# Optimization experiments

Measured on AMD Instinct MI355X. Metric: run time of the kernel, lower is better.

Reference implementation:

```python
import jax, jax.numpy as jnp
import numpy as np

N = 1024
EMB = 128
FC = 512


def setup_inputs() -> dict:
    key = jax.random.key(0)
    ks = jax.random.split(key, 13)
    s = 0.05
    return {
        "x": jax.random.normal(ks[0], (N, 2), jnp.float32),
        "w_rel0": jax.random.normal(ks[1], (EMB, 2), jnp.float32) * s,
        "b_rel0": jax.random.normal(ks[2], (EMB,), jnp.float32) * s,
        "w_root0": jax.random.normal(ks[3], (EMB, 2), jnp.float32) * s,
        "w_rel1": jax.random.normal(ks[4], (EMB, EMB), jnp.float32) * s,
        "b_rel1": jax.random.normal(ks[5], (EMB,), jnp.float32) * s,
        "w_root1": jax.random.normal(ks[6], (EMB, EMB), jnp.float32) * s,
        "lw0": jax.random.normal(ks[7], (FC, EMB), jnp.float32) * s,
        "lb0": jax.random.normal(ks[8], (FC,), jnp.float32) * s,
        "lw1": jax.random.normal(ks[9], (FC, FC), jnp.float32) * s,
        "lb1": jax.random.normal(ks[10], (FC,), jnp.float32) * s,
        "lw2": jax.random.normal(ks[11], (1, FC), jnp.float32) * s,
        "lb2": jax.random.normal(ks[12], (1,), jnp.float32) * s,
    }


def _sage(x, w_rel, b_rel, w_root):
    # DenseSAGEConv with adj = all-ones NxN: neighbor mean == global mean.
    # out = lin_rel(adj@x / deg) + lin_root(x); lin_root has no bias.
    agg = jnp.mean(x, axis=0, keepdims=True)            # (1, d_in)
    return agg @ w_rel.T + b_rel + x @ w_root.T          # (N, d_out)


def reference(x, w_rel0, b_rel0, w_root0, w_rel1, b_rel1, w_root1,
              lw0, lb0, lw1, lb1, lw2, lb2):
    h = jax.nn.relu(_sage(x, w_rel0, b_rel0, w_root0))    # (N, EMB)
    h = jax.nn.relu(_sage(h, w_rel1, b_rel1, w_root1))    # (N, EMB)
    # triu(ones, 1).nonzero() -> all pairs i < j (static, N known at trace time)
    ei, ej = np.triu_indices(h.shape[0], 1)
    e = h[ei] * h[ej]                                     # (E, EMB)
    o = jax.nn.relu(e @ lw0.T + lb0)                      # (E, FC)
    o = jax.nn.relu(o @ lw1.T + lb1)                      # (E, FC)
    o = o @ lw2.T + lb2                                   # (E, 1)
    return jax.nn.sigmoid(o)[:, 0]                        # (E,)
```

## Files before the change

### kernel.cpp

```cpp
#include <hip/hip_runtime.h>
#include <hip/hip_bf16.h>
#include <math.h>

#define NN 1024
#define EMB 128
#define FC 512
#define NEDGE 523776
#define BM 64

typedef __attribute__((ext_vector_type(16))) float f32x16;
typedef __attribute__((ext_vector_type(8))) short bf16x8;
typedef __attribute__((ext_vector_type(4))) unsigned int u32x4;
typedef __attribute__((ext_vector_type(8))) int i32x8;

__device__ __forceinline__ float bf2f(unsigned short u) {
  union { unsigned int i; float f; } v; v.i = ((unsigned int)u) << 16; return v.f;
}
__device__ __forceinline__ unsigned short f2bf(float f) {
  return __builtin_bit_cast(unsigned short, __float2bfloat16(f));
}
__device__ __forceinline__ int cum_edges(int i) { return i * NN - ((i * (i + 1)) >> 1); }

__device__ __forceinline__ unsigned int pk4_fp8(float a, float b, float c, float d) {
  int v = __builtin_amdgcn_cvt_pk_fp8_f32(a, b, 0, false);
  v = __builtin_amdgcn_cvt_pk_fp8_f32(c, d, v, true);
  return (unsigned int)v;
}
#define MFMA32_L0(A,B,C) __builtin_amdgcn_mfma_scale_f32_32x32x64_f8f6f4((A),(B),(C),0,0,0,0x76767676,0,0x7f7f7f7f)
#define MFMA32_L1(A,B,C) __builtin_amdgcn_mfma_scale_f32_32x32x64_f8f6f4((A),(B),(C),0,0,0,0x72727272,0,0x7f7f7f7f)

__global__ void k_cvt_weights(const float* __restrict__ lw0, const float* __restrict__ lw1,
                              unsigned int* __restrict__ w0q, unsigned int* __restrict__ w1q) {
  int d = blockIdx.x * 256 + threadIdx.x;
  if (d < 16384) {
    int dw = d & 7, lane = (d >> 3) & 63, f = (d >> 9) & 1, kb = (d >> 10) & 1, wv = (d >> 11) & 7;
    int fc = wv*64 + f*32 + (lane & 31);
    int k  = kb*64 + (lane >> 5)*32 + dw*4;
    float4 s = *(const float4*)(lw0 + fc*EMB + k);
    w0q[d] = pk4_fp8(s.x*64.f, s.y*64.f, s.z*64.f, s.w*64.f);
  } else {
    int u = d - 16384;
    int dw = u & 7, lane = (u >> 3) & 63, f = (u >> 9) & 1, kb = (u >> 10) & 7, wv = (u >> 13) & 7;
    int fc = wv*64 + f*32 + (lane & 31);
    int k  = kb*64 + (lane >> 5)*32 + dw*4;
    float4 s = *(const float4*)(lw1 + fc*FC + k);
    w1q[u] = pk4_fp8(s.x*64.f, s.y*64.f, s.z*64.f, s.w*64.f);
  }
}

__global__ void k_mean_x(const float* __restrict__ x, float* __restrict__ mean0) {
  __shared__ float sx[256], sy[256];
  float ax = 0.f, ay = 0.f;
  for (int i = threadIdx.x; i < NN; i += 256) { ax += x[2*i]; ay += x[2*i+1]; }
  sx[threadIdx.x] = ax; sy[threadIdx.x] = ay;
  __syncthreads();
  for (int st = 128; st > 0; st >>= 1) {
    if (threadIdx.x < st) { sx[threadIdx.x] += sx[threadIdx.x+st]; sy[threadIdx.x] += sy[threadIdx.x+st]; }
    __syncthreads();
  }
  if (threadIdx.x == 0) { mean0[0] = sx[0] * (1.f/NN); mean0[1] = sy[0] * (1.f/NN); }
}

__global__ void k_sage0(const float* __restrict__ x, const float* __restrict__ wrel,
                        const float* __restrict__ brel, const float* __restrict__ wroot,
                        const float* __restrict__ mean0, float* __restrict__ h0) {
  int idx = blockIdx.x * 256 + threadIdx.x;
  int i = idx >> 7, c = idx & 127;
  float v = mean0[0]*wrel[2*c] + mean0[1]*wrel[2*c+1] + brel[c]
          + x[2*i]*wroot[2*c] + x[2*i+1]*wroot[2*c+1];
  h0[idx] = fmaxf(v, 0.f);
}

__global__ void k_mean_h0(const float* __restrict__ h0, float* __restrict__ mean1) {
  __shared__ float s[256];
  int c = blockIdx.x;
  float a = 0.f;
  for (int i = threadIdx.x; i < NN; i += 256) a += h0[i*EMB + c];
  s[threadIdx.x] = a;
  __syncthreads();
  for (int st = 128; st > 0; st >>= 1) {
    if (threadIdx.x < st) s[threadIdx.x] += s[threadIdx.x+st];
    __syncthreads();
  }
  if (threadIdx.x == 0) mean1[c] = s[0] * (1.f/NN);
}

__global__ void k_relc(const float* __restrict__ mean1, const float* __restrict__ wrel1,
                       const float* __restrict__ brel1, float* __restrict__ relc) {
  int c = threadIdx.x;
  float a = brel1[c];
  #pragma unroll 8
  for (int k = 0; k < EMB; ++k) a += mean1[k] * wrel1[c*EMB + k];
  relc[c] = a;
}

__global__ void k_sage1(const float* __restrict__ h0, const float* __restrict__ wroot1,
                        const float* __restrict__ relc, unsigned short* __restrict__ hb) {
  int idx = blockIdx.x * 256 + threadIdx.x;
  int i = idx >> 7, c = idx & 127;
  const float4* hr = (const float4*)(h0 + i*EMB);
  const float4* wr = (const float4*)(wroot1 + c*EMB);
  float a = relc[c];
  #pragma unroll 8
  for (int k = 0; k < EMB/4; ++k) {
    float4 h = hr[k], w = wr[k];
    a += h.x*w.x + h.y*w.y + h.z*w.z + h.w*w.w;
  }
  hb[idx] = f2bf(fmaxf(a, 0.f) * 32.0f);
}

__global__ __launch_bounds__(512, 4)
void k_edge_mlp(const unsigned short* __restrict__ hb,
                const unsigned int* __restrict__ w0q,
                const float* __restrict__ lb0,
                const unsigned int* __restrict__ w1q,
                const float* __restrict__ lb1,
                const float* __restrict__ lw2,
                const float* __restrict__ lb2,
                float* __restrict__ out) {
  __shared__ __align__(16) unsigned int e_lds[2048];
  __shared__ __align__(16) unsigned int o0_lds[8192];

  const int tid  = threadIdx.x;
  const int lane = tid & 63;
  const int wv   = tid >> 6;
  const int l31  = lane & 31;
  const int hi   = lane >> 5;
  const int blk  = blockIdx.x;
  const int fcb  = wv * 64;

  const char* w0w = (const char*)w0q + wv * 8192;
  const char* w1w = (const char*)w1q + wv * 32768;

  {
    int r = tid >> 3, q = tid & 7;
    int k = blk * BM + r;
    float s = sqrtf((float)(4190209 - 8*k));
    int i = (int)((2047.0f - s) * 0.5f);
    if (i < 0) i = 0;
    if (i > NN-2) i = NN-2;
    if (cum_edges(i+1) <= k) ++i;
    if (cum_edges(i+1) <= k) ++i;
    if (cum_edges(i) > k) --i;
    if (cum_edges(i) > k) --i;
    int j = k - cum_edges(i) + i + 1;
    const bf16x8* hi8 = (const bf16x8*)(hb + i*EMB + q*16);
    const bf16x8* hj8 = (const bf16x8*)(hb + j*EMB + q*16);
    float p[16];
    #pragma unroll
    for (int g = 0; g < 2; ++g) {
      bf16x8 a = hi8[g], b = hj8[g];
      #pragma unroll
      for (int u = 0; u < 8; ++u)
        p[g*8+u] = bf2f((unsigned short)a[u]) * bf2f((unsigned short)b[u]);
    }
    u32x4 d;
    #pragma unroll
    for (int u = 0; u < 4; ++u)
      d[u] = pk4_fp8(p[4*u], p[4*u+1], p[4*u+2], p[4*u+3]);
    int byt = (r>>5)*4096 + (q>>2)*2048 + (q&1)*1024 + (((q>>1)&1)*32 + (r&31))*16;
    *(u32x4*)((char*)e_lds + byt) = d;
  }
  __syncthreads();

  f32x16 acc[2][2];

  #pragma unroll
  for (int f = 0; f < 2; ++f)
    #pragma unroll
    for (int t = 0; t < 4; ++t) {
      float4 bv = *(const float4*)(lb0 + fcb + f*32 + t*8 + hi*4);
      #pragma unroll
      for (int e = 0; e < 2; ++e) {
        acc[e][f][4*t+0] = bv.x*128.f; acc[e][f][4*t+1] = bv.y*128.f;
        acc[e][f][4*t+2] = bv.z*128.f; acc[e][f][4*t+3] = bv.w*128.f;
      }
    }
  {
    const char* rbe = (const char*)e_lds + lane*16;
    #pragma unroll
    for (int kb = 0; kb < 2; ++kb) {
      i32x8 a0 = *(const i32x8*)(w0w + (kb*2+0)*2048 + lane*32);
      i32x8 a1 = *(const i32x8*)(w0w + (kb*2+1)*2048 + lane*32);
      i32x8 b0, b1;
      *(u32x4*)&b0       = *(const u32x4*)(rbe + kb*2048);
      *((u32x4*)&b0 + 1) = *(const u32x4*)(rbe + kb*2048 + 1024);
      *(u32x4*)&b1       = *(const u32x4*)(rbe + 4096 + kb*2048);
      *((u32x4*)&b1 + 1) = *(const u32x4*)(rbe + 4096 + kb*2048 + 1024);
      __builtin_amdgcn_s_setprio(1);
      acc[0][0] = MFMA32_L0(a0, b0, acc[0][0]);
      acc[0][1] = MFMA32_L0(a1, b0, acc[0][1]);
      acc[1][0] = MFMA32_L0(a0, b1, acc[1][0]);
      acc[1][1] = MFMA32_L0(a1, b1, acc[1][1]);
      __builtin_amdgcn_s_setprio(0);
    }
  }

  {
    char* ob = (char*)o0_lds + wv*2048 + l31*16 + hi*4;
    #pragma unroll
    for (int f = 0; f < 2; ++f)
      #pragma unroll
      for (int e = 0; e < 2; ++e)
        #pragma unroll
        for (int t = 0; t < 4; ++t) {
          unsigned int d = pk4_fp8(fmaxf(acc[e][f][4*t+0], 0.f),
                                   fmaxf(acc[e][f][4*t+1], 0.f),
                                   fmaxf(acc[e][f][4*t+2], 0.f),
                                   fmaxf(acc[e][f][4*t+3], 0.f));
          *(unsigned int*)(ob + e*16384 + (t>>1)*1024 + f*512 + (t&1)*8) = d;
        }
  }
  __syncthreads();

  #pragma unroll
  for (int f = 0; f < 2; ++f)
    #pragma unroll
    for (int t = 0; t < 4; ++t) {
      float4 bv = *(const float4*)(lb1 + fcb + f*32 + t*8 + hi*4);
      #pragma unroll
      for (int e = 0; e < 2; ++e) {
        acc[e][f][4*t+0] = bv.x; acc[e][f][4*t+1] = bv.y;
        acc[e][f][4*t+2] = bv.z; acc[e][f][4*t+3] = bv.w;
      }
    }
  {
    const char* rbo = (const char*)o0_lds + lane*16;
    #pragma unroll
    for (int kb = 0; kb < 8; ++kb) {
      i32x8 a0 = *(const i32x8*)(w1w + (kb*2+0)*2048 + lane*32);
      i32x8 a1 = *(const i32x8*)(w1w + (kb*2+1)*2048 + lane*32);
      i32x8 b0, b1;
      *(u32x4*)&b0       = *(const u32x4*)(rbo + kb*2048);
      *((u32x4*)&b0 + 1) = *(const u32x4*)(rbo + kb*2048 + 1024);
      *(u32x4*)&b1       = *(const u32x4*)(rbo + 16384 + kb*2048);
      *((u32x4*)&b1 + 1) = *(const u32x4*)(rbo + 16384 + kb*2048 + 1024);
      __builtin_amdgcn_s_setprio(1);
      acc[0][0] = MFMA32_L1(a0, b0, acc[0][0]);
      acc[0][1] = MFMA32_L1(a1, b0, acc[0][1]);
      acc[1][0] = MFMA32_L1(a0, b1, acc[1][0]);
      acc[1][1] = MFMA32_L1(a1, b1, acc[1][1]);
      __builtin_amdgcn_s_setprio(0);
    }
  }

  {
    float rs0 = 0.f, rs1 = 0.f;
    #pragma unroll
    for (int f = 0; f < 2; ++f)
      #pragma unroll
      for (int t = 0; t < 4; ++t) {
        float4 l2v = *(const float4*)(lw2 + fcb + f*32 + t*8 + hi*4);
        rs0 += fmaxf(acc[0][f][4*t+0], 0.f) * l2v.x;
        rs0 += fmaxf(acc[0][f][4*t+1], 0.f) * l2v.y;
        rs0 += fmaxf(acc[0][f][4*t+2], 0.f) * l2v.z;
        rs0 += fmaxf(acc[0][f][4*t+3], 0.f) * l2v.w;
        rs1 += fmaxf(acc[1][f][4*t+0], 0.f) * l2v.x;
        rs1 += fmaxf(acc[1][f][4*t+1], 0.f) * l2v.y;
        rs1 += fmaxf(acc[1][f][4*t+2], 0.f) * l2v.z;
        rs1 += fmaxf(acc[1][f][4*t+3], 0.f) * l2v.w;
      }
    rs0 += __shfl_xor(rs0, 32, 64);
    rs1 += __shfl_xor(rs1, 32, 64);
    float* red = (float*)e_lds;
    if (hi == 0) {
      red[wv*64 + l31]      = rs0;
      red[wv*64 + 32 + l31] = rs1;
    }
  }
  __syncthreads();

  if (tid < BM) {
    const float* red = (const float*)e_lds;
    float v = lb2[0];
    #pragma unroll
    for (int w = 0; w < 8; ++w) v += red[w*BM + tid];
    out[blk*BM + tid] = 1.0f / (1.0f + __expf(-v));
  }
}

extern "C" void kernel_launch(void* const* d_in, const int* in_sizes, int n_in,
                              void* d_out, int out_size, void* d_ws, size_t ws_size,
                              hipStream_t stream) {
  const float* x      = (const float*)d_in[0];
  const float* wrel0  = (const float*)d_in[1];
  const float* brel0  = (const float*)d_in[2];
  const float* wroot0 = (const float*)d_in[3];
  const float* wrel1  = (const float*)d_in[4];
  const float* brel1  = (const float*)d_in[5];
  const float* wroot1 = (const float*)d_in[6];
  const float* lw0    = (const float*)d_in[7];
  const float* lb0    = (const float*)d_in[8];
  const float* lw1    = (const float*)d_in[9];
  const float* lb1    = (const float*)d_in[10];
  const float* lw2    = (const float*)d_in[11];
  const float* lb2    = (const float*)d_in[12];
  float* out = (float*)d_out;

  char* ws = (char*)d_ws;
  unsigned short* hb  = (unsigned short*)(ws);
  unsigned int*   w0q = (unsigned int*)(ws + 262144);
  unsigned int*   w1q = (unsigned int*)(ws + 327680);
  float* h0    = (float*)(ws + 589824);
  float* mean0 = (float*)(ws + 1114112);
  float* mean1 = (float*)(ws + 1114176);
  float* relc  = (float*)(ws + 1114688);

  hipLaunchKernelGGL(k_cvt_weights, dim3(320), dim3(256), 0, stream, lw0, lw1, w0q, w1q);
  hipLaunchKernelGGL(k_mean_x,   dim3(1),    dim3(256), 0, stream, x, mean0);
  hipLaunchKernelGGL(k_sage0,    dim3(512),  dim3(256), 0, stream, x, wrel0, brel0, wroot0, mean0, h0);
  hipLaunchKernelGGL(k_mean_h0,  dim3(128),  dim3(256), 0, stream, h0, mean1);
  hipLaunchKernelGGL(k_relc,     dim3(1),    dim3(128), 0, stream, mean1, wrel1, brel1, relc);
  hipLaunchKernelGGL(k_sage1,    dim3(512),  dim3(256), 0, stream, h0, wroot1, relc, hb);
  hipLaunchKernelGGL(k_edge_mlp, dim3(NEDGE/BM), dim3(512), 0, stream,
                     hb, w0q, lb0, w1q, lb1, lw2, lb2, out);
}
```

Baseline: 198.0 us.

## Double edge tile to 128 rows per block and restructure MFMA loops

Raises edges per block from 64 to 128, doubling the LDS staging buffers. Each wave now holds four edge sub-tiles and loops over the two FC halves sequentially, so each weight fragment loaded from global memory is reused across four MFMAs instead of two. This halves per-edge weight traffic and block count, at the cost of more LDS per block (80KB), which may cut occupancy, and a longer serial loop per block.

```diff
diff --git a/kernel.cpp b/kernel.cpp
--- a/kernel.cpp
+++ b/kernel.cpp
@@ -6,7 +6,7 @@
 #define EMB 128
 #define FC 512
 #define NEDGE 523776
-#define BM 64
+#define BM 128
 
 typedef __attribute__((ext_vector_type(16))) float f32x16;
 typedef __attribute__((ext_vector_type(8))) short bf16x8;
@@ -118,8 +118,8 @@
                 const float* __restrict__ lw2,
                 const float* __restrict__ lb2,
                 float* __restrict__ out) {
-  __shared__ __align__(16) unsigned int e_lds[2048];
-  __shared__ __align__(16) unsigned int o0_lds[8192];
+  __shared__ __align__(16) unsigned int e_lds[4096];
+  __shared__ __align__(16) unsigned int o0_lds[16384];
 
   const int tid  = threadIdx.x;
   const int lane = tid & 63;
@@ -133,7 +133,8 @@
   const char* w1w = (const char*)w1q + wv * 32768;
 
   {
-    int r = tid >> 3, q = tid & 7;
+    int r = tid >> 2;
+    int c4 = tid & 3;
     int k = blk * BM + r;
     float s = sqrtf((float)(4190209 - 8*k));
     int i = (int)((2047.0f - s) * 0.5f);
@@ -144,128 +145,131 @@
     if (cum_edges(i) > k) --i;
     if (cum_edges(i) > k) --i;
     int j = k - cum_edges(i) + i + 1;
-    const bf16x8* hi8 = (const bf16x8*)(hb + i*EMB + q*16);
-    const bf16x8* hj8 = (const bf16x8*)(hb + j*EMB + q*16);
-    float p[16];
+    const bf16x8* hi8 = (const bf16x8*)(hb + i*EMB + c4*32);
+    const bf16x8* hj8 = (const bf16x8*)(hb + j*EMB + c4*32);
+    int base = (r>>5)*4096 + (c4>>1)*2048 + ((c4&1)*32 + (r&31))*16;
     #pragma unroll
     for (int g = 0; g < 2; ++g) {
-      bf16x8 a = hi8[g], b = hj8[g];
-      #pragma unroll
-      for (int u = 0; u < 8; ++u)
-        p[g*8+u] = bf2f((unsigned short)a[u]) * bf2f((unsigned short)b[u]);
+      bf16x8 a0 = hi8[g*2], a1 = hi8[g*2+1];
+      bf16x8 b0 = hj8[g*2], b1 = hj8[g*2+1];
+      float p[16];
+      #pragma unroll
+      for (int u = 0; u < 8; ++u) {
+        p[u]   = bf2f((unsigned short)a0[u]) * bf2f((unsigned short)b0[u]);
+        p[8+u] = bf2f((unsigned short)a1[u]) * bf2f((unsigned short)b1[u]);
+      }
+      u32x4 d;
+      #pragma unroll
+      for (int u = 0; u < 4; ++u)
+        d[u] = pk4_fp8(p[4*u], p[4*u+1], p[4*u+2], p[4*u+3]);
+      *(u32x4*)((char*)e_lds + base + g*1024) = d;
     }
-    u32x4 d;
-    #pragma unroll
-    for (int u = 0; u < 4; ++u)
-      d[u] = pk4_fp8(p[4*u], p[4*u+1], p[4*u+2], p[4*u+3]);
-    int byt = (r>>5)*4096 + (q>>2)*2048 + (q&1)*1024 + (((q>>1)&1)*32 + (r&31))*16;
-    *(u32x4*)((char*)e_lds + byt) = d;
-  }
-  __syncthreads();
-
-  f32x16 acc[2][2];
-
-  #pragma unroll
-  for (int f = 0; f < 2; ++f)
-    #pragma unroll
-    for (int t = 0; t < 4; ++t) {
-      float4 bv = *(const float4*)(lb0 + fcb + f*32 + t*8 + hi*4);
-      #pragma unroll
-      for (int e = 0; e < 2; ++e) {
-        acc[e][f][4*t+0] = bv.x*128.f; acc[e][f][4*t+1] = bv.y*128.f;
-        acc[e][f][4*t+2] = bv.z*128.f; acc[e][f][4*t+3] = bv.w*128.f;
-      }
-    }
+  }
+  __syncthreads();
+
   {
     const char* rbe = (const char*)e_lds + lane*16;
-    #pragma unroll
-    for (int kb = 0; kb < 2; ++kb) {
-      i32x8 a0 = *(const i32x8*)(w0w + (kb*2+0)*2048 + lane*32);
-      i32x8 a1 = *(const i32x8*)(w0w + (kb*2+1)*2048 + lane*32);
-      i32x8 b0, b1;
-      *(u32x4*)&b0       = *(const u32x4*)(rbe + kb*2048);
-      *((u32x4*)&b0 + 1) = *(const u32x4*)(rbe + kb*2048 + 1024);
-      *(u32x4*)&b1       = *(const u32x4*)(rbe + 4096 + kb*2048);
-      *((u32x4*)&b1 + 1) = *(const u32x4*)(rbe + 4096 + kb*2048 + 1024);
-      __builtin_amdgcn_s_setprio(1);
-      acc[0][0] = MFMA32_L0(a0, b0, acc[0][0]);
-      acc[0][1] = MFMA32_L0(a1, b0, acc[0][1]);
-      acc[1][0] = MFMA32_L0(a0, b1, acc[1][0]);
-      acc[1][1] = MFMA32_L0(a1, b1, acc[1][1]);
-      __builtin_amdgcn_s_setprio(0);
-    }
-  }
-
-  {
     char* ob = (char*)o0_lds + wv*2048 + l31*16 + hi*4;
     #pragma unroll
-    for (int f = 0; f < 2; ++f)
-      #pragma unroll
-      for (int e = 0; e < 2; ++e)
+    for (int f = 0; f < 2; ++f) {
+      f32x16 acc[4];
+      #pragma unroll
+      for (int t = 0; t < 4; ++t) {
+        float4 bv = *(const float4*)(lb0 + fcb + f*32 + t*8 + hi*4);
+        #pragma unroll
+        for (int e = 0; e < 4; ++e) {
+          acc[e][4*t+0] = bv.x*128.f; acc[e][4*t+1] = bv.y*128.f;
+          acc[e][4*t+2] = bv.z*128.f; acc[e][4*t+3] = bv.w*128.f;
+        }
+      }
+      #pragma unroll
+      for (int kb = 0; kb < 2; ++kb) {
+        i32x8 aw = *(const i32x8*)(w0w + (kb*2+f)*2048 + lane*32);
+        i32x8 b0, b1, b2, b3;
+        *(u32x4*)&b0       = *(const u32x4*)(rbe + 0*4096 + kb*2048);
+        *((u32x4*)&b0 + 1) = *(const u32x4*)(rbe + 0*4096 + kb*2048 + 1024);
+        *(u32x4*)&b1       = *(const u32x4*)(rbe + 1*4096 + kb*2048);
+        *((u32x4*)&b1 + 1) = *(const u32x4*)(rbe + 1*4096 + kb*2048 + 1024);
+        *(u32x4*)&b2       = *(const u32x4*)(rbe + 2*4096 + kb*2048);
+        *((u32x4*)&b2 + 1) = *(const u32x4*)(rbe + 2*4096 + kb*2048 + 1024);
+        *(u32x4*)&b3       = *(const u32x4*)(rbe + 3*4096 + kb*2048);
+        *((u32x4*)&b3 + 1) = *(const u32x4*)(rbe + 3*4096 + kb*2048 + 1024);
+        __builtin_amdgcn_s_setprio(1);
+        acc[0] = MFMA32_L0(aw, b0, acc[0]);
+        acc[1] = MFMA32_L0(aw, b1, acc[1]);
+        acc[2] = MFMA32_L0(aw, b2, acc[2]);
+        acc[3] = MFMA32_L0(aw, b3, acc[3]);
+        __builtin_amdgcn_s_setprio(0);
+      }
+      #pragma unroll
+      for (int e = 0; e < 4; ++e)
         #pragma unroll
         for (int t = 0; t < 4; ++t) {
-          unsigned int d = pk4_fp8(fmaxf(acc[e][f][4*t+0], 0.f),
-                                   fmaxf(acc[e][f][4*t+1], 0.f),
-                                   fmaxf(acc[e][f][4*t+2], 0.f),
-                                   fmaxf(acc[e][f][4*t+3], 0.f));
+          unsigned int d = pk4_fp8(fmaxf(acc[e][4*t+0], 0.f),
+                                   fmaxf(acc[e][4*t+1], 0.f),
+                                   fmaxf(acc[e][4*t+2], 0.f),
+                                   fmaxf(acc[e][4*t+3], 0.f));
           *(unsigned int*)(ob + e*16384 + (t>>1)*1024 + f*512 + (t&1)*8) = d;
         }
-  }
-  __syncthreads();
-
-  #pragma unroll
-  for (int f = 0; f < 2; ++f)
-    #pragma unroll
-    for (int t = 0; t < 4; ++t) {
-      float4 bv = *(const float4*)(lb1 + fcb + f*32 + t*8 + hi*4);
-      #pragma unroll
-      for (int e = 0; e < 2; ++e) {
-        acc[e][f][4*t+0] = bv.x; acc[e][f][4*t+1] = bv.y;
-        acc[e][f][4*t+2] = bv.z; acc[e][f][4*t+3] = bv.w;
-      }
     }
+  }
+  __syncthreads();
+
+  float rs[4] = {0.f, 0.f, 0.f, 0.f};
   {
     const char* rbo = (const char*)o0_lds + lane*16;
     #pragma unroll
-    for (int kb = 0; kb < 8; ++kb) {
-      i32x8 a0 = *(const i32x8*)(w1w + (kb*2+0)*2048 + lane*32);
-      i32x8 a1 = *(const i32x8*)(w1w + (kb*2+1)*2048 + lane*32);
-      i32x8 b0, b1;
-      *(u32x4*)&b0       = *(const u32x4*)(rbo + kb*2048);
-      *((u32x4*)&b0 + 1) = *(const u32x4*)(rbo + kb*2048 + 1024);
-      *(u32x4*)&b1       = *(const u32x4*)(rbo + 16384 + kb*2048);
-      *((u32x4*)&b1 + 1) = *(const u32x4*)(rbo + 16384 + kb*2048 + 1024);
-      __builtin_amdgcn_s_setprio(1);
-      acc[0][0] = MFMA32_L1(a0, b0, acc[0][0]);
-      acc[0][1] = MFMA32_L1(a1, b0, acc[0][1]);
-      acc[1][0] = MFMA32_L1(a0, b1, acc[1][0]);
-      acc[1][1] = MFMA32_L1(a1, b1, acc[1][1]);
-      __builtin_amdgcn_s_setprio(0);
-    }
-  }
-
-  {
-    float rs0 = 0.f, rs1 = 0.f;
-    #pragma unroll
-    for (int f = 0; f < 2; ++f)
+    for (int f = 0; f < 2; ++f) {
+      f32x16 acc[4];
+      #pragma unroll
+      for (int t = 0; t < 4; ++t) {
+        float4 bv = *(const float4*)(lb1 + fcb + f*32 + t*8 + hi*4);
+        #pragma unroll
+        for (int e = 0; e < 4; ++e) {
+          acc[e][4*t+0] = bv.x; acc[e][4*t+1] = bv.y;
+          acc[e][4*t+2] = bv.z; acc[e][4*t+3] = bv.w;
+        }
+      }
+      #pragma unroll
+      for (int kb = 0; kb < 8; ++kb) {
+        i32x8 aw = *(const i32x8*)(w1w + (kb*2+f)*2048 + lane*32);
+        i32x8 b0, b1, b2, b3;
+        *(u32x4*)&b0       = *(const u32x4*)(rbo + 0*16384 + kb*2048);
+        *((u32x4*)&b0 + 1) = *(const u32x4*)(rbo + 0*16384 + kb*2048 + 1024);
+        *(u32x4*)&b1       = *(const u32x4*)(rbo + 1*16384 + kb*2048);
+        *((u32x4*)&b1 + 1) = *(const u32x4*)(rbo + 1*16384 + kb*2048 + 1024);
+        *(u32x4*)&b2       = *(const u32x4*)(rbo + 2*16384 + kb*2048);
+        *((u32x4*)&b2 + 1) = *(const u32x4*)(rbo + 2*16384 + kb*2048 + 1024);
+        *(u32x4*)&b3       = *(const u32x4*)(rbo + 3*16384 + kb*2048);
+        *((u32x4*)&b3 + 1) = *(const u32x4*)(rbo + 3*16384 + kb*2048 + 1024);
+        __builtin_amdgcn_s_setprio(1);
+        acc[0] = MFMA32_L1(aw, b0, acc[0]);
+        acc[1] = MFMA32_L1(aw, b1, acc[1]);
+        acc[2] = MFMA32_L1(aw, b2, acc[2]);
+        acc[3] = MFMA32_L1(aw, b3, acc[3]);
+        __builtin_amdgcn_s_setprio(0);
+      }
       #pragma unroll
       for (int t = 0; t < 4; ++t) {
         float4 l2v = *(const float4*)(lw2 + fcb + f*32 + t*8 + hi*4);
-        rs0 += fmaxf(acc[0][f][4*t+0], 0.f) * l2v.x;
-        rs0 += fmaxf(acc[0][f][4*t+1], 0.f) * l2v.y;
-        rs0 += fmaxf(acc[0][f][4*t+2], 0.f) * l2v.z;
-        rs0 += fmaxf(acc[0][f][4*t+3], 0.f) * l2v.w;
-        rs1 += fmaxf(acc[1][f][4*t+0], 0.f) * l2v.x;
-        rs1 += fmaxf(acc[1][f][4*t+1], 0.f) * l2v.y;
-        rs1 += fmaxf(acc[1][f][4*t+2], 0.f) * l2v.z;
-        rs1 += fmaxf(acc[1][f][4*t+3], 0.f) * l2v.w;
-      }
-    rs0 += __shfl_xor(rs0, 32, 64);
-    rs1 += __shfl_xor(rs1, 32, 64);
+        #pragma unroll
+        for (int e = 0; e < 4; ++e) {
+          rs[e] += fmaxf(acc[e][4*t+0], 0.f) * l2v.x;
+          rs[e] += fmaxf(acc[e][4*t+1], 0.f) * l2v.y;
+          rs[e] += fmaxf(acc[e][4*t+2], 0.f) * l2v.z;
+          rs[e] += fmaxf(acc[e][4*t+3], 0.f) * l2v.w;
+        }
+      }
+    }
+  }
+
+  {
+    #pragma unroll
+    for (int e = 0; e < 4; ++e) rs[e] += __shfl_xor(rs[e], 32, 64);
     float* red = (float*)e_lds;
     if (hi == 0) {
-      red[wv*64 + l31]      = rs0;
-      red[wv*64 + 32 + l31] = rs1;
+      #pragma unroll
+      for (int e = 0; e < 4; ++e) red[wv*BM + e*32 + l31] = rs[e];
     }
   }
   __syncthreads();
```

New measurement: 781.6 us. +294.7%, slower.
